# Performance work log

Measured on AMD Instinct MI355X. Metric: run time of the kernel, lower is better.

## Reference

```python
import jax, jax.numpy as jnp
import numpy as np

B, NP, C, NS = 32, 192, 128, 36
MID, FCH = 64, 128
RH, RW = 10, 25
FH, FW = 40, 100
EPS = 1e-5

def _bn(x, g, b, m, v, axis=1):
    shape = [1] * x.ndim; shape[axis] = -1
    g, b, m, v = (t.reshape(shape) for t in (g, b, m, v))
    return g * (x - m) * jax.lax.rsqrt(v + EPS) + b

def _conv9(x, w):
    # x: (N, Cin, L), w: (Cout, Cin, 9), 'same' pad 4 -- torch Conv2d (9,1) on (N,C,Ns,1)
    return jax.lax.conv_general_dilated(x, w, (1,), ((4, 4),), dimension_numbers=('NCH', 'OIH', 'NCH'))

def _resize_nearest(x):
    # torch F.interpolate(mode='nearest'): src = floor(dst * in / out); then flatten(2)
    Bx, Cx, H, W = x.shape
    hi = jnp.arange(RH) * H // RH
    wi = jnp.arange(RW) * W // RW
    return x[:, :, hi][:, :, :, wi].reshape(Bx, Cx, RH * RW)

def setup_inputs():
    key = jax.random.key(0)
    ks = jax.random.split(key, 40)
    rn = lambda i, s, sc=1.0: jax.random.normal(ks[i], s, jnp.float32) * sc
    ru = lambda i, s: jax.random.uniform(ks[i], s, jnp.float32)
    return dict(
        roi_feat0=rn(0, (B * NP, C, NS, 1)), roi_feat1=rn(1, (B * NP, C, NS, 1)), roi_feat2=rn(2, (B * NP, C, NS, 1)),
        fmap=rn(3, (B, C, FH, FW)),
        conv_w=rn(4, (3, MID, C, 9), (C * 9) ** -0.5),
        conv_g=jnp.ones((3, MID)), conv_b=jnp.zeros((3, MID)),
        conv_m=rn(5, (3, MID), 0.1), conv_v=1.0 + 0.1 * ru(6, (3, MID)),
        cat_w=rn(7, (C, 3 * MID, 9), (3 * MID * 9) ** -0.5),
        cat_g=jnp.ones((C,)), cat_b=jnp.zeros((C,)),
        cat_m=rn(8, (C,), 0.1), cat_v=1.0 + 0.1 * ru(9, (C,)),
        fc_w=rn(10, (FCH, NS * C), (NS * C) ** -0.5), fc_b=rn(11, (FCH,), 0.01),
        ln_g=jnp.ones((FCH,)), ln_b=jnp.zeros((FCH,)),
        key_w=rn(12, (C, C), C ** -0.5),
        key_g=jnp.ones((C,)), key_beta=jnp.zeros((C,)),
        key_m=rn(13, (C,), 0.1), key_v=1.0 + 0.1 * ru(14, (C,)),
        q_w=1.0 + 0.1 * rn(15, (NP,)), q_b=rn(16, (NP,), 0.01),
        val_w=rn(17, (C, C), C ** -0.5), val_b=rn(18, (C,), 0.01),
        gate_w=rn(19, (NP,), 0.1), gate_b=rn(20, (NP,), 0.01),
        layer_index=2,
    )

def reference(roi_feat0, roi_feat1, roi_feat2, fmap, conv_w, conv_g, conv_b, conv_m, conv_v,
              cat_w, cat_g, cat_b, cat_m, cat_v, fc_w, fc_b, ln_g, ln_b,
              key_w, key_g, key_beta, key_m, key_v, q_w, q_b, val_w, val_b, gate_w, gate_b,
              layer_index):
    relu = jax.nn.relu
    # roi_fea: per-level 9x1 ConvModule (conv+BN+ReLU), concat, catconv at layer_index (=2 here)
    rois = [roi_feat0[..., 0], roi_feat1[..., 0], roi_feat2[..., 0]]  # (B*NP, C, NS)
    feats = [relu(_bn(_conv9(r, conv_w[i]), conv_g[i], conv_b[i], conv_m[i], conv_v[i]))
             for i, r in enumerate(rois)]
    cat = jnp.concatenate(feats, axis=1)                              # (B*NP, 3*MID, NS)
    cat = relu(_bn(_conv9(cat, cat_w), cat_g, cat_b, cat_m, cat_v))    # (B*NP, C, NS)
    # fc + LayerNorm + ReLU; torch .view flattens C-major then NS
    flat = cat.reshape(B * NP, C * NS)
    h = flat @ fc_w.T + fc_b
    mu = h.mean(-1, keepdims=True)
    var = ((h - mu) ** 2).mean(-1, keepdims=True)
    roi = relu((h - mu) * jax.lax.rsqrt(var + EPS) * ln_g + ln_b).reshape(B, NP, FCH)
    # AnchorVecFeatureMapAttention
    q = relu(roi * q_w[None, :, None] + q_b[None, :, None])           # grouped 1x1 conv1d == per-prior affine
    kmap = relu(_bn(jnp.einsum('oc,bchw->bohw', key_w, fmap), key_g, key_beta, key_m, key_v))
    k = _resize_nearest(kmap)                                          # (B, C, 250)
    v = _resize_nearest(jnp.einsum('oc,bchw->bohw', val_w, fmap) + val_b[None, :, None, None])
    v = v.transpose(0, 2, 1)                                           # (B, 250, C)
    sim = jax.nn.softmax(jnp.einsum('bnc,bcl->bnl', q, k) * C ** -0.5, axis=-1)
    ctx = jnp.einsum('bnl,blc->bnc', sim, v)
    ctx = ctx * gate_w[None, :, None] + gate_b[None, :, None]          # grouped W conv
    return roi + ctx  # cross_attention_weight=1.0; dropout identity in eval
```

## Files before the change

### kernel.cpp

```cpp
#include <hip/hip_runtime.h>

#define B_   32
#define NP_  192
#define C_   128
#define NS_  36
#define MID_ 64
#define FCH_ 128
#define RH_  10
#define RW_  25
#define FH_  40
#define FW_  100
#define L_   250
#define NR_  (B_*NP_)
#define EPS_ 1e-5f

#define G_    4
#define XROWS 44
#define CPX   136
#define CPC   200

typedef _Float16 f16;
typedef f16   f16x8 __attribute__((ext_vector_type(8)));
typedef f16   f16x4 __attribute__((ext_vector_type(4)));
typedef float f32x4 __attribute__((ext_vector_type(4)));

#define MFMA16(a,b,c) __builtin_amdgcn_mfma_f32_16x16x32_f16((a),(b),(c),0,0,0)

#define WS_KBUF   0u
#define WS_VBUF   4096000u
#define WS_CONVWT 8192000u
#define WS_CATWT  (WS_CONVWT + 442368u)
#define WS_FCWH   (WS_CATWT + 442368u)

__global__ __launch_bounds__(256) void k_prep(
    const float* __restrict__ conv_w, const float* __restrict__ cat_w,
    const float* __restrict__ fc_w,
    f16* __restrict__ cwt, f16* __restrict__ kwt, f16* __restrict__ fwh)
{
  int i = blockIdx.x * 256 + threadIdx.x;
  if (i < 221184) {
    int cin = i & 127;
    int r   = i >> 7;
    int oc  = r & 63; r >>= 6;
    int tap = r % 9, lev = r / 9;
    cwt[i] = (f16)conv_w[(((size_t)(lev*64 + oc))*128 + cin)*9 + tap];
  } else if (i < 442368) {
    int j   = i - 221184;
    int cin = j % 192;
    int r   = j / 192;
    int oc  = r & 127;
    int tap = r >> 7;
    kwt[j] = (f16)cat_w[((size_t)oc*192 + cin)*9 + tap];
  } else if (i < 1032192) {
    int k = i - 442368;
    fwh[k] = (f16)fc_w[k];
  }
}

__global__ __launch_bounds__(512) void k_roi(
    const float* __restrict__ rf0, const float* __restrict__ rf1, const float* __restrict__ rf2,
    const f16* __restrict__ cwt, const f16* __restrict__ kwt, const f16* __restrict__ fwh,
    const float* __restrict__ cg, const float* __restrict__ cb,
    const float* __restrict__ cm, const float* __restrict__ cv,
    const float* __restrict__ wg, const float* __restrict__ wb,
    const float* __restrict__ wm, const float* __restrict__ wvv,
    const float* __restrict__ fcb, const float* __restrict__ lng, const float* __restrict__ lnb,
    float* __restrict__ roi)
{
  __shared__ __align__(16) char smem[122368];
  f16*   Xt  = (f16*)smem;
  f16*   Yh  = (f16*)smem;
  f16*   cst = (f16*)(smem + 47872);
  float* scr = (float*)(smem + 118272);
  float* hs  = (float*)(smem + 120320);

  const int tid  = threadIdx.x, lane = tid & 63, w = tid >> 6;
  const int r16  = lane & 15, g4 = lane >> 4;
  const int nbase = blockIdx.x * G_;

  for (int i = tid; i < G_*8*CPX; i += 512) {
    int rr = i / CPX, col = i - rr*CPX;
    int g = rr >> 3, r8 = rr & 7;
    int row = (r8 < 4) ? r8 : (36 + r8);
    Xt[(g*XROWS + row)*CPX + col] = (f16)0.f;
  }
  for (int i = tid; i < G_*8*CPC; i += 512) {
    int rr = i / CPC, col = i - rr*CPC;
    int g = rr >> 3, r8 = rr & 7;
    int row = (r8 < 4) ? r8 : (36 + r8);
    cst[(g*XROWS + row)*CPC + col] = (f16)0.f;
  }

  const int mh = w & 1, nq = w >> 1;
  const int nNT = (nq == 0) ? 3 : 2;
  int xoff[3], coffR[3], coffW[3], gq[3], sq[3];
  #pragma unroll
  for (int nl = 0; nl < 3; nl++) {
    int nt = nq + 4*nl; if (nt > 8) nt = 8;
    int q = nt*16 + r16;
    int g = q / 36, s = q - 36*g;
    gq[nl] = g; sq[nl] = s;
    xoff[nl]  = (g*XROWS + s)*CPX + g4*8;
    coffR[nl] = (g*XROWS + s)*CPC + g4*8;
    coffW[nl] = (g*XROWS + 4 + s)*CPC;
  }

  for (int lev = 0; lev < 3; lev++) {
    {
      int g = tid >> 7, t = tid & 127;
      const float* src = (lev == 0 ? rf0 : (lev == 1 ? rf1 : rf2))
                         + (size_t)(nbase + g) * (C_*NS_);
      for (int it = 0; it < 9; it++) {
        int idx = t + 128*it;
        int c = idx / 9, s4 = (idx - 9*c)*4;
        float4 v = *(const float4*)(src + c*NS_ + s4);
        f16* dst = Xt + (g*XROWS + 4 + s4)*CPX + c;
        dst[0*CPX] = (f16)v.x; dst[1*CPX] = (f16)v.y;
        dst[2*CPX] = (f16)v.z; dst[3*CPX] = (f16)v.w;
      }
    }
    __syncthreads();

    f32x4 acc[2][3];
    #pragma unroll
    for (int ml = 0; ml < 2; ml++)
      #pragma unroll
      for (int nl = 0; nl < 3; nl++) { f32x4 z = {0.f,0.f,0.f,0.f}; acc[ml][nl] = z; }

    const f16* wl = cwt + (size_t)lev*9*64*128;
    for (int ks = 0; ks < 36; ks++) {
      int tap = ks >> 2, c0 = (ks & 3) << 5;
      const f16* wt = wl + tap*(64*128) + r16*128 + c0 + g4*8;
      f16x8 a0 = *(const f16x8*)(wt + (2*mh+0)*16*128);
      f16x8 a1 = *(const f16x8*)(wt + (2*mh+1)*16*128);
      int xo = tap*CPX + c0;
      f16x8 b0 = *(const f16x8*)(Xt + xoff[0] + xo);
      f16x8 b1 = *(const f16x8*)(Xt + xoff[1] + xo);
      acc[0][0] = MFMA16(a0, b0, acc[0][0]);
      acc[1][0] = MFMA16(a1, b0, acc[1][0]);
      acc[0][1] = MFMA16(a0, b1, acc[0][1]);
      acc[1][1] = MFMA16(a1, b1, acc[1][1]);
      if (nNT == 3) {
        f16x8 b2 = *(const f16x8*)(Xt + xoff[2] + xo);
        acc[0][2] = MFMA16(a0, b2, acc[0][2]);
        acc[1][2] = MFMA16(a1, b2, acc[1][2]);
      }
    }

    #pragma unroll
    for (int ml = 0; ml < 2; ml++) {
      int mt  = 2*mh + ml;
      int ocl = mt*16 + g4*4;
      int ocg = lev*64 + ocl;
      float sc[4], sh[4];
      #pragma unroll
      for (int r = 0; r < 4; r++) {
        float s0 = cg[ocg+r] * rsqrtf(cv[ocg+r] + EPS_);
        sc[r] = s0; sh[r] = cb[ocg+r] - cm[ocg+r]*s0;
      }
      #pragma unroll
      for (int nl = 0; nl < 3; nl++) if (nl < nNT) {
        f16x4 o;
        #pragma unroll
        for (int r = 0; r < 4; r++)
          o[r] = (f16)fmaxf(fmaf(sc[r], acc[ml][nl][r], sh[r]), 0.f);
        *(f16x4*)(cst + coffW[nl] + lev*64 + ocl) = o;
      }
    }
    __syncthreads();
  }

  {
    f32x4 acc[4][3];
    #pragma unroll
    for (int ml = 0; ml < 4; ml++)
      #pragma unroll
      for (int nl = 0; nl < 3; nl++) { f32x4 z = {0.f,0.f,0.f,0.f}; acc[ml][nl] = z; }

    int tap = 0, c6 = 0;
    for (int ks = 0; ks < 54; ks++) {
      int c0 = c6 << 5;
      const f16* wt = kwt + (size_t)(tap*128 + 4*mh*16 + r16)*192 + c0 + g4*8;
      f16x8 a0 = *(const f16x8*)(wt + 0*16*192);
      f16x8 a1 = *(const f16x8*)(wt + 1*16*192);
      f16x8 a2 = *(const f16x8*)(wt + 2*16*192);
      f16x8 a3 = *(const f16x8*)(wt + 3*16*192);
      int co = tap*CPC + c0;
      f16x8 b0 = *(const f16x8*)(cst + coffR[0] + co);
      f16x8 b1 = *(const f16x8*)(cst + coffR[1] + co);
      acc[0][0] = MFMA16(a0, b0, acc[0][0]);
      acc[1][0] = MFMA16(a1, b0, acc[1][0]);
      acc[2][0] = MFMA16(a2, b0, acc[2][0]);
      acc[3][0] = MFMA16(a3, b0, acc[3][0]);
      acc[0][1] = MFMA16(a0, b1, acc[0][1]);
      acc[1][1] = MFMA16(a1, b1, acc[1][1]);
      acc[2][1] = MFMA16(a2, b1, acc[2][1]);
      acc[3][1] = MFMA16(a3, b1, acc[3][1]);
      if (nNT == 3) {
        f16x8 b2 = *(const f16x8*)(cst + coffR[2] + co);
        acc[0][2] = MFMA16(a0, b2, acc[0][2]);
        acc[1][2] = MFMA16(a1, b2, acc[1][2]);
        acc[2][2] = MFMA16(a2, b2, acc[2][2]);
        acc[3][2] = MFMA16(a3, b2, acc[3][2]);
      }
      if (++c6 == 6) { c6 = 0; tap++; }
    }

    #pragma unroll
    for (int ml = 0; ml < 4; ml++) {
      int oc0 = (4*mh + ml)*16 + g4*4;
      float sc[4], sh[4];
      #pragma unroll
      for (int r = 0; r < 4; r++) {
        float s0 = wg[oc0+r] * rsqrtf(wvv[oc0+r] + EPS_);
        sc[r] = s0; sh[r] = wb[oc0+r] - wm[oc0+r]*s0;
      }
      #pragma unroll
      for (int nl = 0; nl < 3; nl++) if (nl < nNT) {
        int yb = gq[nl]*4608 + oc0*36 + sq[nl];
        #pragma unroll
        for (int r = 0; r < 4; r++)
          Yh[yb + r*36] = (f16)fmaxf(fmaf(sc[r], acc[ml][nl][r], sh[r]), 0.f);
      }
    }
  }
  __syncthreads();

  {
    const int mtp = w & 3, kh = w >> 2;
    const int gcol = r16 & 3;
    f32x4 fa0 = {0.f,0.f,0.f,0.f}, fa1 = fa0;
    const f16* bb0 = Yh + gcol*4608 + kh*2304 + g4*8;
    const f16* aw0 = fwh + (size_t)((2*mtp+0)*16 + r16)*4608 + kh*2304 + g4*8;
    const f16* aw1 = fwh + (size_t)((2*mtp+1)*16 + r16)*4608 + kh*2304 + g4*8;
    for (int ks = 0; ks < 72; ks++) {
      int k0 = ks*32;
      f16x8 bb = *(const f16x8*)(bb0 + k0);
      f16x8 a0 = *(const f16x8*)(aw0 + k0);
      f16x8 a1 = *(const f16x8*)(aw1 + k0);
      fa0 = MFMA16(a0, bb, fa0);
      fa1 = MFMA16(a1, bb, fa1);
    }
    if (kh == 1 && r16 < 4) {
      #pragma unroll
      for (int r = 0; r < 4; r++) {
        scr[((2*mtp+0)*16 + g4*4 + r)*4 + r16] = fa0[r];
        scr[((2*mtp+1)*16 + g4*4 + r)*4 + r16] = fa1[r];
      }
    }
    __syncthreads();
    if (kh == 0 && r16 < 4) {
      #pragma unroll
      for (int r = 0; r < 4; r++) {
        int f0 = (2*mtp+0)*16 + g4*4 + r;
        int f1 = (2*mtp+1)*16 + g4*4 + r;
        hs[r16*128 + f0] = fa0[r] + scr[f0*4 + r16] + fcb[f0];
        hs[r16*128 + f1] = fa1[r] + scr[f1*4 + r16] + fcb[f1];
      }
    }
  }
  __syncthreads();

  {
    int g = w >> 1, f = (w & 1)*64 + lane;
    float h = hs[g*128 + f];
    float s1 = h, s2 = h*h;
    #pragma unroll
    for (int off = 32; off; off >>= 1) {
      s1 += __shfl_xor(s1, off, 64);
      s2 += __shfl_xor(s2, off, 64);
    }
    if (lane == 0) { scr[w*2] = s1; scr[w*2+1] = s2; }
    __syncthreads();
    float S1 = scr[(2*g)*2]   + scr[(2*g+1)*2];
    float S2 = scr[(2*g)*2+1] + scr[(2*g+1)*2+1];
    float mu  = S1 * (1.f/128.f);
    float var = S2 * (1.f/128.f) - mu*mu;
    float rr  = rsqrtf(var + EPS_);
    roi[(size_t)(nbase + g)*FCH_ + f] = fmaxf((h - mu)*rr*lng[f] + lnb[f], 0.f);
  }
}

__global__ __launch_bounds__(128) void k_kv(
    const float* __restrict__ fmap,
    const float* __restrict__ kw, const float* __restrict__ kg, const float* __restrict__ kbeta,
    const float* __restrict__ km, const float* __restrict__ kvv,
    const float* __restrict__ vw, const float* __restrict__ vb,
    float* __restrict__ kbuf, float* __restrict__ vbuf)
{
  int l = blockIdx.x, b = blockIdx.y, tid = threadIdx.x;
  int r = l / RW_, s = l % RW_;
  int pix = (r * FH_ / RH_) * FW_ + (s * FW_ / RW_);
  __shared__ float fs[C_];
  fs[tid] = fmap[((size_t)b * C_ + tid) * (FH_ * FW_) + pix];
  __syncthreads();

  int c = tid;
  const float4* kwp = reinterpret_cast<const float4*>(kw + (size_t)c * C_);
  const float4* vwp = reinterpret_cast<const float4*>(vw + (size_t)c * C_);
  float kk = 0.f, vv = 0.f;
  for (int i = 0; i < 32; i++) {
    float4 ku = kwp[i]; float4 vu = vwp[i];
    const float* fb = fs + i * 4;
    kk = fmaf(ku.x, fb[0], kk);  vv = fmaf(vu.x, fb[0], vv);
    kk = fmaf(ku.y, fb[1], kk);  vv = fmaf(vu.y, fb[1], vv);
    kk = fmaf(ku.z, fb[2], kk);  vv = fmaf(vu.z, fb[2], vv);
    kk = fmaf(ku.w, fb[3], kk);  vv = fmaf(vu.w, fb[3], vv);
  }
  float scale = kg[c] * rsqrtf(kvv[c] + EPS_);
  float shift = kbeta[c] - km[c] * scale;
  kbuf[((size_t)b * C_ + c) * L_ + l] = fmaxf(fmaf(scale, kk, shift), 0.f);
  vbuf[((size_t)b * L_ + l) * C_ + c] = vv + vb[c];
}

__global__ __launch_bounds__(256) void k_attn(
    const float* __restrict__ kbuf, const float* __restrict__ vbuf,
    const float* __restrict__ qw, const float* __restrict__ qb,
    const float* __restrict__ gw, const float* __restrict__ gb,
    float* __restrict__ out)
{
  int nglob = blockIdx.x;
  int b = nglob / NP_, np = nglob % NP_;
  int tid = threadIdx.x;
  __shared__ float qs[C_];
  __shared__ float ps[256];
  __shared__ float rbuf[8];

  float* rp = out + (size_t)nglob * C_;
  if (tid < C_) qs[tid] = fmaxf(fmaf(rp[tid], qw[np], qb[np]), 0.f);
  __syncthreads();

  float sc = -1e30f;
  if (tid < L_) {
    const float* kp = kbuf + (size_t)b * (C_ * L_) + tid;
    float a = 0.f;
    for (int c = 0; c < C_; c++) a = fmaf(qs[c], kp[c * L_], a);
    sc = a * 0.088388347648318447f;
  }
  float m = sc;
  #pragma unroll
  for (int off = 32; off; off >>= 1) m = fmaxf(m, __shfl_xor(m, off, 64));
  if ((tid & 63) == 0) rbuf[tid >> 6] = m;
  __syncthreads();
  m = fmaxf(fmaxf(rbuf[0], rbuf[1]), fmaxf(rbuf[2], rbuf[3]));

  float e = (tid < L_) ? __expf(sc - m) : 0.f;
  ps[tid] = e;
  float s = e;
  #pragma unroll
  for (int off = 32; off; off >>= 1) s += __shfl_xor(s, off, 64);
  if ((tid & 63) == 0) rbuf[4 + (tid >> 6)] = s;
  __syncthreads();
  float S = rbuf[4] + rbuf[5] + rbuf[6] + rbuf[7];
  float inv = 1.f / S;

  if (tid < C_) {
    const float* vp = vbuf + (size_t)b * (L_ * C_) + tid;
    float a = 0.f;
    for (int l = 0; l < L_; l++) a = fmaf(ps[l], vp[l * C_], a);
    a *= inv;
    rp[tid] = rp[tid] + a * gw[np] + gb[np];
  }
}

extern "C" void kernel_launch(void* const* d_in, const int* in_sizes, int n_in,
                              void* d_out, int out_size, void* d_ws, size_t ws_size,
                              hipStream_t stream)
{
  const float* rf0    = (const float*)d_in[0];
  const float* rf1    = (const float*)d_in[1];
  const float* rf2    = (const float*)d_in[2];
  const float* fmap   = (const float*)d_in[3];
  const float* conv_w = (const float*)d_in[4];
  const float* conv_g = (const float*)d_in[5];
  const float* conv_b = (const float*)d_in[6];
  const float* conv_m = (const float*)d_in[7];
  const float* conv_v = (const float*)d_in[8];
  const float* cat_w  = (const float*)d_in[9];
  const float* cat_g  = (const float*)d_in[10];
  const float* cat_b  = (const float*)d_in[11];
  const float* cat_m  = (const float*)d_in[12];
  const float* cat_v  = (const float*)d_in[13];
  const float* fc_w   = (const float*)d_in[14];
  const float* fc_b   = (const float*)d_in[15];
  const float* ln_g   = (const float*)d_in[16];
  const float* ln_b   = (const float*)d_in[17];
  const float* key_w  = (const float*)d_in[18];
  const float* key_g  = (const float*)d_in[19];
  const float* key_be = (const float*)d_in[20];
  const float* key_m  = (const float*)d_in[21];
  const float* key_v  = (const float*)d_in[22];
  const float* q_w    = (const float*)d_in[23];
  const float* q_b    = (const float*)d_in[24];
  const float* val_w  = (const float*)d_in[25];
  const float* val_b  = (const float*)d_in[26];
  const float* gate_w = (const float*)d_in[27];
  const float* gate_b = (const float*)d_in[28];

  float* roi  = (float*)d_out;
  char*  ws   = (char*)d_ws;
  float* kbuf = (float*)(ws + WS_KBUF);
  float* vbuf = (float*)(ws + WS_VBUF);
  f16*   cwt  = (f16*)(ws + WS_CONVWT);
  f16*   kwt  = (f16*)(ws + WS_CATWT);
  f16*   fwh  = (f16*)(ws + WS_FCWH);

  k_prep<<<dim3(4032), 256, 0, stream>>>(conv_w, cat_w, fc_w, cwt, kwt, fwh);
  k_kv<<<dim3(L_, B_), 128, 0, stream>>>(fmap, key_w, key_g, key_be, key_m, key_v,
                                         val_w, val_b, kbuf, vbuf);
  k_roi<<<dim3(NR_/G_), 512, 0, stream>>>(rf0, rf1, rf2, cwt, kwt, fwh,
                                          conv_g, conv_b, conv_m, conv_v,
                                          cat_g, cat_b, cat_m, cat_v,
                                          fc_b, ln_g, ln_b, roi);
  k_attn<<<dim3(NR_), 256, 0, stream>>>(kbuf, vbuf, q_w, q_b, gate_w, gate_b, roi);
}
```

Baseline: 1.350 ms.

## Batch attention on MFMA with fp16 K/V, vectorize ROI loads, unroll conv loops

The attention kernel is rewritten to handle 32 priors per block. It uses MFMA for QK^T and PV, with K and V stored as transposed fp16 padded to 256 positions, replacing the per-prior scalar fp32 dot-product loops. The ROI feature transpose-load now reads four channel rows per thread and writes packed f16x4 into shared memory. The conv and fc MFMA loops are templated on tile count and fully or partially unrolled. Storing K, V and probabilities in fp16 lowers precision, and heavier unrolling may raise register pressure in the 512-thread kernel.

```diff
diff --git a/kernel.cpp b/kernel.cpp
--- a/kernel.cpp
+++ b/kernel.cpp
@@ -26,9 +26,9 @@
 
 #define MFMA16(a,b,c) __builtin_amdgcn_mfma_f32_16x16x32_f16((a),(b),(c),0,0,0)
 
-#define WS_KBUF   0u
-#define WS_VBUF   4096000u
-#define WS_CONVWT 8192000u
+#define WS_KT     0u
+#define WS_VT     2097152u
+#define WS_CONVWT 4194304u
 #define WS_CATWT  (WS_CONVWT + 442368u)
 #define WS_FCWH   (WS_CATWT + 442368u)
 
@@ -57,6 +57,64 @@
   }
 }
 
+template<int NNT>
+__device__ __forceinline__ void s1_loop(const f16* __restrict__ wl, const f16* Xt,
+    int xoff0, int xoff1, int xoff2, int mh, int r16, int g4, f32x4 acc[2][3])
+{
+  #pragma unroll
+  for (int ks = 0; ks < 36; ks++) {
+    const int tap = ks >> 2, c0 = (ks & 3) << 5;
+    const f16* wt = wl + tap*(64*128) + r16*128 + c0 + g4*8;
+    f16x8 a0 = *(const f16x8*)(wt + (2*mh+0)*16*128);
+    f16x8 a1 = *(const f16x8*)(wt + (2*mh+1)*16*128);
+    const int xo = tap*CPX + c0;
+    f16x8 b0 = *(const f16x8*)(Xt + xoff0 + xo);
+    f16x8 b1 = *(const f16x8*)(Xt + xoff1 + xo);
+    acc[0][0] = MFMA16(a0, b0, acc[0][0]);
+    acc[1][0] = MFMA16(a1, b0, acc[1][0]);
+    acc[0][1] = MFMA16(a0, b1, acc[0][1]);
+    acc[1][1] = MFMA16(a1, b1, acc[1][1]);
+    if (NNT == 3) {
+      f16x8 b2 = *(const f16x8*)(Xt + xoff2 + xo);
+      acc[0][2] = MFMA16(a0, b2, acc[0][2]);
+      acc[1][2] = MFMA16(a1, b2, acc[1][2]);
+    }
+  }
+}
+
+template<int NNT>
+__device__ __forceinline__ void s2_loop(const f16* __restrict__ kwt, const f16* cst,
+    int co0, int co1, int co2, int mh, int r16, int g4, f32x4 acc[4][3])
+{
+  #pragma unroll 18
+  for (int ks = 0; ks < 54; ks++) {
+    const int tap = ks / 6, c0 = (ks % 6) << 5;
+    const f16* wt = kwt + (size_t)(tap*128 + 4*mh*16 + r16)*192 + c0 + g4*8;
+    f16x8 a0 = *(const f16x8*)(wt + 0*16*192);
+    f16x8 a1 = *(const f16x8*)(wt + 1*16*192);
+    f16x8 a2 = *(const f16x8*)(wt + 2*16*192);
+    f16x8 a3 = *(const f16x8*)(wt + 3*16*192);
+    const int co = tap*CPC + c0;
+    f16x8 b0 = *(const f16x8*)(cst + co0 + co);
+    f16x8 b1 = *(const f16x8*)(cst + co1 + co);
+    acc[0][0] = MFMA16(a0, b0, acc[0][0]);
+    acc[1][0] = MFMA16(a1, b0, acc[1][0]);
+    acc[2][0] = MFMA16(a2, b0, acc[2][0]);
+    acc[3][0] = MFMA16(a3, b0, acc[3][0]);
+    acc[0][1] = MFMA16(a0, b1, acc[0][1]);
+    acc[1][1] = MFMA16(a1, b1, acc[1][1]);
+    acc[2][1] = MFMA16(a2, b1, acc[2][1]);
+    acc[3][1] = MFMA16(a3, b1, acc[3][1]);
+    if (NNT == 3) {
+      f16x8 b2 = *(const f16x8*)(cst + co2 + co);
+      acc[0][2] = MFMA16(a0, b2, acc[0][2]);
+      acc[1][2] = MFMA16(a1, b2, acc[1][2]);
+      acc[2][2] = MFMA16(a2, b2, acc[2][2]);
+      acc[3][2] = MFMA16(a3, b2, acc[3][2]);
+    }
+  }
+}
+
 __global__ __launch_bounds__(512) void k_roi(
     const float* __restrict__ rf0, const float* __restrict__ rf1, const float* __restrict__ rf2,
     const f16* __restrict__ cwt, const f16* __restrict__ kwt, const f16* __restrict__ fwh,
@@ -107,16 +165,25 @@
 
   for (int lev = 0; lev < 3; lev++) {
     {
-      int g = tid >> 7, t = tid & 127;
-      const float* src = (lev == 0 ? rf0 : (lev == 1 ? rf1 : rf2))
-                         + (size_t)(nbase + g) * (C_*NS_);
-      for (int it = 0; it < 9; it++) {
-        int idx = t + 128*it;
-        int c = idx / 9, s4 = (idx - 9*c)*4;
-        float4 v = *(const float4*)(src + c*NS_ + s4);
-        f16* dst = Xt + (g*XROWS + 4 + s4)*CPX + c;
-        dst[0*CPX] = (f16)v.x; dst[1*CPX] = (f16)v.y;
-        dst[2*CPX] = (f16)v.z; dst[3*CPX] = (f16)v.w;
+      const float* rfl = (lev == 0 ? rf0 : (lev == 1 ? rf1 : rf2));
+      #pragma unroll
+      for (int it = 0; it < 3; it++) {
+        int item = tid + 512*it;
+        if (item < 1152) {
+          int g  = item / 288, rem = item - 288*g;
+          int cb = rem / 9,  sb = rem - 9*cb;
+          const float* src = rfl + (size_t)(nbase + g)*(C_*NS_) + (4*cb)*NS_ + 4*sb;
+          float4 v0 = *(const float4*)(src + 0*NS_);
+          float4 v1 = *(const float4*)(src + 1*NS_);
+          float4 v2 = *(const float4*)(src + 2*NS_);
+          float4 v3 = *(const float4*)(src + 3*NS_);
+          f16* db = Xt + (g*XROWS + 4 + 4*sb)*CPX + 4*cb;
+          f16x4 o;
+          o[0]=(f16)v0.x; o[1]=(f16)v1.x; o[2]=(f16)v2.x; o[3]=(f16)v3.x; *(f16x4*)(db + 0*CPX) = o;
+          o[0]=(f16)v0.y; o[1]=(f16)v1.y; o[2]=(f16)v2.y; o[3]=(f16)v3.y; *(f16x4*)(db + 1*CPX) = o;
+          o[0]=(f16)v0.z; o[1]=(f16)v1.z; o[2]=(f16)v2.z; o[3]=(f16)v3.z; *(f16x4*)(db + 2*CPX) = o;
+          o[0]=(f16)v0.w; o[1]=(f16)v1.w; o[2]=(f16)v2.w; o[3]=(f16)v3.w; *(f16x4*)(db + 3*CPX) = o;
+        }
       }
     }
     __syncthreads();
@@ -128,24 +195,8 @@
       for (int nl = 0; nl < 3; nl++) { f32x4 z = {0.f,0.f,0.f,0.f}; acc[ml][nl] = z; }
 
     const f16* wl = cwt + (size_t)lev*9*64*128;
-    for (int ks = 0; ks < 36; ks++) {
-      int tap = ks >> 2, c0 = (ks & 3) << 5;
-      const f16* wt = wl + tap*(64*128) + r16*128 + c0 + g4*8;
-      f16x8 a0 = *(const f16x8*)(wt + (2*mh+0)*16*128);
-      f16x8 a1 = *(const f16x8*)(wt + (2*mh+1)*16*128);
-      int xo = tap*CPX + c0;
-      f16x8 b0 = *(const f16x8*)(Xt + xoff[0] + xo);
-      f16x8 b1 = *(const f16x8*)(Xt + xoff[1] + xo);
-      acc[0][0] = MFMA16(a0, b0, acc[0][0]);
-      acc[1][0] = MFMA16(a1, b0, acc[1][0]);
-      acc[0][1] = MFMA16(a0, b1, acc[0][1]);
-      acc[1][1] = MFMA16(a1, b1, acc[1][1]);
-      if (nNT == 3) {
-        f16x8 b2 = *(const f16x8*)(Xt + xoff[2] + xo);
-        acc[0][2] = MFMA16(a0, b2, acc[0][2]);
-        acc[1][2] = MFMA16(a1, b2, acc[1][2]);
-      }
-    }
+    if (nNT == 3) s1_loop<3>(wl, Xt, xoff[0], xoff[1], xoff[2], mh, r16, g4, acc);
+    else          s1_loop<2>(wl, Xt, xoff[0], xoff[1], xoff[2], mh, r16, g4, acc);
 
     #pragma unroll
     for (int ml = 0; ml < 2; ml++) {
@@ -177,34 +228,8 @@
       #pragma unroll
       for (int nl = 0; nl < 3; nl++) { f32x4 z = {0.f,0.f,0.f,0.f}; acc[ml][nl] = z; }
 
-    int tap = 0, c6 = 0;
-    for (int ks = 0; ks < 54; ks++) {
-      int c0 = c6 << 5;
-      const f16* wt = kwt + (size_t)(tap*128 + 4*mh*16 + r16)*192 + c0 + g4*8;
-      f16x8 a0 = *(const f16x8*)(wt + 0*16*192);
-      f16x8 a1 = *(const f16x8*)(wt + 1*16*192);
-      f16x8 a2 = *(const f16x8*)(wt + 2*16*192);
-      f16x8 a3 = *(const f16x8*)(wt + 3*16*192);
-      int co = tap*CPC + c0;
-      f16x8 b0 = *(const f16x8*)(cst + coffR[0] + co);
-      f16x8 b1 = *(const f16x8*)(cst + coffR[1] + co);
-      acc[0][0] = MFMA16(a0, b0, acc[0][0]);
-      acc[1][0] = MFMA16(a1, b0, acc[1][0]);
-      acc[2][0] = MFMA16(a2, b0, acc[2][0]);
-      acc[3][0] = MFMA16(a3, b0, acc[3][0]);
-      acc[0][1] = MFMA16(a0, b1, acc[0][1]);
-      acc[1][1] = MFMA16(a1, b1, acc[1][1]);
-      acc[2][1] = MFMA16(a2, b1, acc[2][1]);
-      acc[3][1] = MFMA16(a3, b1, acc[3][1]);
-      if (nNT == 3) {
-        f16x8 b2 = *(const f16x8*)(cst + coffR[2] + co);
-        acc[0][2] = MFMA16(a0, b2, acc[0][2]);
-        acc[1][2] = MFMA16(a1, b2, acc[1][2]);
-        acc[2][2] = MFMA16(a2, b2, acc[2][2]);
-        acc[3][2] = MFMA16(a3, b2, acc[3][2]);
-      }
-      if (++c6 == 6) { c6 = 0; tap++; }
-    }
+    if (nNT == 3) s2_loop<3>(kwt, cst, coffR[0], coffR[1], coffR[2], mh, r16, g4, acc);
+    else          s2_loop<2>(kwt, cst, coffR[0], coffR[1], coffR[2], mh, r16, g4, acc);
 
     #pragma unroll
     for (int ml = 0; ml < 4; ml++) {
@@ -233,6 +258,7 @@
     const f16* bb0 = Yh + gcol*4608 + kh*2304 + g4*8;
     const f16* aw0 = fwh + (size_t)((2*mtp+0)*16 + r16)*4608 + kh*2304 + g4*8;
     const f16* aw1 = fwh + (size_t)((2*mtp+1)*16 + r16)*4608 + kh*2304 + g4*8;
+    #pragma unroll
     for (int ks = 0; ks < 72; ks++) {
       int k0 = ks*32;
       f16x8 bb = *(const f16x8*)(bb0 + k0);
@@ -286,9 +312,14 @@
     const float* __restrict__ kw, const float* __restrict__ kg, const float* __restrict__ kbeta,
     const float* __restrict__ km, const float* __restrict__ kvv,
     const float* __restrict__ vw, const float* __restrict__ vb,
-    float* __restrict__ kbuf, float* __restrict__ vbuf)
+    f16* __restrict__ kT, f16* __restrict__ vT)
 {
   int l = blockIdx.x, b = blockIdx.y, tid = threadIdx.x;
+  if (l >= L_) {
+    kT[((size_t)b*256 + l)*C_ + tid] = (f16)0.f;
+    vT[((size_t)b*C_ + tid)*256 + l] = (f16)0.f;
+    return;
+  }
   int r = l / RW_, s = l % RW_;
   int pix = (r * FH_ / RH_) * FW_ + (s * FW_ / RW_);
   __shared__ float fs[C_];
@@ -309,57 +340,120 @@
   }
   float scale = kg[c] * rsqrtf(kvv[c] + EPS_);
   float shift = kbeta[c] - km[c] * scale;
-  kbuf[((size_t)b * C_ + c) * L_ + l] = fmaxf(fmaf(scale, kk, shift), 0.f);
-  vbuf[((size_t)b * L_ + l) * C_ + c] = vv + vb[c];
+  kT[((size_t)b*256 + l)*C_ + c] = (f16)fmaxf(fmaf(scale, kk, shift), 0.f);
+  vT[((size_t)b*C_ + c)*256 + l] = (f16)(vv + vb[c]);
 }
 
 __global__ __launch_bounds__(256) void k_attn(
-    const float* __restrict__ kbuf, const float* __restrict__ vbuf,
+    const f16* __restrict__ kT, const f16* __restrict__ vT,
     const float* __restrict__ qw, const float* __restrict__ qb,
     const float* __restrict__ gw, const float* __restrict__ gb,
     float* __restrict__ out)
 {
-  int nglob = blockIdx.x;
-  int b = nglob / NP_, np = nglob % NP_;
-  int tid = threadIdx.x;
-  __shared__ float qs[C_];
-  __shared__ float ps[256];
-  __shared__ float rbuf[8];
-
-  float* rp = out + (size_t)nglob * C_;
-  if (tid < C_) qs[tid] = fmaxf(fmaf(rp[tid], qw[np], qb[np]), 0.f);
+  int qt = blockIdx.x, b = blockIdx.y;
+  int np0 = qt * 32;
+  int tid = threadIdx.x, lane = tid & 63, w = tid >> 6;
+  int r16 = lane & 15, g4 = lane >> 4;
+
+  __shared__ __align__(16) f16   qA[32*136];
+  __shared__ __align__(16) float S[32*264];
+  __shared__ __align__(16) f16   P[32*264];
+  __shared__ float sinv[32];
+
+  {
+    int m = tid >> 3, c0 = (tid & 7) * 16;
+    int np = np0 + m;
+    const float* rp = out + ((size_t)b*NP_ + np)*C_ + c0;
+    float aa = qw[np], bb = qb[np];
+    f16* dst = qA + m*136 + c0;
+    #pragma unroll
+    for (int j = 0; j < 16; j++) dst[j] = (f16)fmaxf(fmaf(rp[j], aa, bb), 0.f);
+  }
   __syncthreads();
 
-  float sc = -1e30f;
-  if (tid < L_) {
-    const float* kp = kbuf + (size_t)b * (C_ * L_) + tid;
-    float a = 0.f;
-    for (int c = 0; c < C_; c++) a = fmaf(qs[c], kp[c * L_], a);
-    sc = a * 0.088388347648318447f;
-  }
-  float m = sc;
-  #pragma unroll
-  for (int off = 32; off; off >>= 1) m = fmaxf(m, __shfl_xor(m, off, 64));
-  if ((tid & 63) == 0) rbuf[tid >> 6] = m;
+  const f16* kTb = kT + (size_t)b*256*C_;
+  const f16* vTb = vT + (size_t)b*C_*256;
+
+  {
+    int mt = w & 1, ntg = w >> 1;
+    f32x4 acc[8];
+    #pragma unroll
+    for (int j = 0; j < 8; j++) { f32x4 z = {0.f,0.f,0.f,0.f}; acc[j] = z; }
+    #pragma unroll
+    for (int ks = 0; ks < 4; ks++) {
+      f16x8 a = *(const f16x8*)(qA + (mt*16 + r16)*136 + ks*32 + g4*8);
+      #pragma unroll
+      for (int j = 0; j < 8; j++) {
+        int nt = ntg*8 + j;
+        f16x8 bf = *(const f16x8*)(kTb + (size_t)(nt*16 + r16)*C_ + ks*32 + g4*8);
+        acc[j] = MFMA16(a, bf, acc[j]);
+      }
+    }
+    #pragma unroll
+    for (int j = 0; j < 8; j++) {
+      int nt = ntg*8 + j;
+      #pragma unroll
+      for (int r = 0; r < 4; r++)
+        S[(mt*16 + g4*4 + r)*264 + nt*16 + r16] = acc[j][r];
+    }
+  }
   __syncthreads();
-  m = fmaxf(fmaxf(rbuf[0], rbuf[1]), fmaxf(rbuf[2], rbuf[3]));
-
-  float e = (tid < L_) ? __expf(sc - m) : 0.f;
-  ps[tid] = e;
-  float s = e;
-  #pragma unroll
-  for (int off = 32; off; off >>= 1) s += __shfl_xor(s, off, 64);
-  if ((tid & 63) == 0) rbuf[4 + (tid >> 6)] = s;
+
+  {
+    int row = tid >> 3, sub = tid & 7;
+    const float sc = 0.088388347648318447f;
+    float v[32];
+    float mx = -1e30f;
+    #pragma unroll
+    for (int k = 0; k < 32; k++) {
+      int n = sub + 8*k;
+      float x = (n < L_) ? S[row*264 + n]*sc : -1e30f;
+      v[k] = x;
+      mx = fmaxf(mx, x);
+    }
+    #pragma unroll
+    for (int off = 1; off < 8; off <<= 1) mx = fmaxf(mx, __shfl_xor(mx, off, 64));
+    float s = 0.f;
+    #pragma unroll
+    for (int k = 0; k < 32; k++) {
+      int n = sub + 8*k;
+      float e = (n < L_) ? __expf(v[k] - mx) : 0.f;
+      P[row*264 + n] = (f16)e;
+      s += e;
+    }
+    #pragma unroll
+    for (int off = 1; off < 8; off <<= 1) s += __shfl_xor(s, off, 64);
+    if (sub == 0) sinv[row] = 1.f / s;
+  }
   __syncthreads();
-  float S = rbuf[4] + rbuf[5] + rbuf[6] + rbuf[7];
-  float inv = 1.f / S;
-
-  if (tid < C_) {
-    const float* vp = vbuf + (size_t)b * (L_ * C_) + tid;
-    float a = 0.f;
-    for (int l = 0; l < L_; l++) a = fmaf(ps[l], vp[l * C_], a);
-    a *= inv;
-    rp[tid] = rp[tid] + a * gw[np] + gb[np];
+
+  {
+    int mt = w & 1, ntg = w >> 1;
+    f32x4 acc[4];
+    #pragma unroll
+    for (int j = 0; j < 4; j++) { f32x4 z = {0.f,0.f,0.f,0.f}; acc[j] = z; }
+    #pragma unroll
+    for (int ks = 0; ks < 8; ks++) {
+      f16x8 a = *(const f16x8*)(P + (mt*16 + r16)*264 + ks*32 + g4*8);
+      #pragma unroll
+      for (int j = 0; j < 4; j++) {
+        int nt = ntg*4 + j;
+        f16x8 bf = *(const f16x8*)(vTb + (size_t)(nt*16 + r16)*256 + ks*32 + g4*8);
+        acc[j] = MFMA16(a, bf, acc[j]);
+      }
+    }
+    #pragma unroll
+    for (int r = 0; r < 4; r++) {
+      int m = mt*16 + g4*4 + r;
+      int np = np0 + m;
+      float gwv = gw[np], gbv = gb[np], si = sinv[m];
+      float* rp = out + ((size_t)b*NP_ + np)*C_;
+      #pragma unroll
+      for (int j = 0; j < 4; j++) {
+        int c = (ntg*4 + j)*16 + r16;
+        rp[c] = rp[c] + acc[j][r]*si*gwv + gbv;
+      }
+    }
   }
 }
 
@@ -399,18 +493,18 @@
 
   float* roi  = (float*)d_out;
   char*  ws   = (char*)d_ws;
-  float* kbuf = (float*)(ws + WS_KBUF);
-  float* vbuf = (float*)(ws + WS_VBUF);
+  f16*   kT   = (f16*)(ws + WS_KT);
+  f16*   vT   = (f16*)(ws + WS_VT);
   f16*   cwt  = (f16*)(ws + WS_CONVWT);
   f16*   kwt  = (f16*)(ws + WS_CATWT);
   f16*   fwh  = (f16*)(ws + WS_FCWH);
 
   k_prep<<<dim3(4032), 256, 0, stream>>>(conv_w, cat_w, fc_w, cwt, kwt, fwh);
-  k_kv<<<dim3(L_, B_), 128, 0, stream>>>(fmap, key_w, key_g, key_be, key_m, key_v,
-                                         val_w, val_b, kbuf, vbuf);
+  k_kv<<<dim3(256, B_), 128, 0, stream>>>(fmap, key_w, key_g, key_be, key_m, key_v,
+                                          val_w, val_b, kT, vT);
   k_roi<<<dim3(NR_/G_), 512, 0, stream>>>(rf0, rf1, rf2, cwt, kwt, fwh,
                                           conv_g, conv_b, conv_m, conv_v,
                                           cat_g, cat_b, cat_m, cat_v,
                                           fc_b, ln_g, ln_b, roi);
-  k_attn<<<dim3(NR_), 256, 0, stream>>>(kbuf, vbuf, q_w, q_b, gate_w, gate_b, roi);
-}
+  k_attn<<<dim3(6, B_), 256, 0, stream>>>(kT, vT, q_w, q_b, gate_w, gate_b, roi);
+}
```

Result: faster. 1.297 ms (-3.9%).
